# Kernel optimization log

Measured on AMD Instinct MI355X. Metric: run time of the kernel, lower is better.

Reference implementation:

```python
import jax, jax.numpy as jnp
import numpy as np

B, H, W, K, A = 4096, 32, 32, 20, 4


def setup_inputs() -> dict:
    key = jax.random.key(0)
    k_wall, k_agent, k_goal, k_phi, k_l1, k_l2 = jax.random.split(key, 6)
    # obs channels: 0 = wall/feature map (random), 1 = one-hot agent pos, 2 = one-hot goal pos
    walls = jax.random.uniform(k_wall, (B, H, W), dtype=jnp.float32)
    agent_idx = jax.random.randint(k_agent, (B,), 0, H * W)
    goal_idx = jax.random.randint(k_goal, (B,), 0, H * W)
    agent = jax.nn.one_hot(agent_idx, H * W, dtype=jnp.float32).reshape(B, H, W)
    goal = jax.nn.one_hot(goal_idx, H * W, dtype=jnp.float32).reshape(B, H, W)
    obs = jnp.stack([walls, agent, goal], axis=-1)  # (B,H,W,3)
    obs_flat = obs.reshape(B, H * W * 3)
    din = H * W * 3
    return {
        "obs_flat": obs_flat,
        "Phi_w": jax.random.normal(k_phi, (din, 2 * H * W), dtype=jnp.float32) * 0.02,
        "Phi_b": jnp.zeros((2 * H * W,), jnp.float32),
        "L1_w": jax.random.normal(k_l1, (36, 16), dtype=jnp.float32) * 0.1,
        "L1_b": jnp.zeros((16,), jnp.float32),
        "L2_w": jax.random.normal(k_l2, (16, A), dtype=jnp.float32) * 0.1,
        "L2_b": jnp.zeros((A,), jnp.float32),
    }


def _mvprop(r, p):
    # K-step value propagation: V <- max(V, r + p*(best 4-neighbor V - r))
    # p = sigmoid(...) >= 0, so max over the 4 shifted nv values equals nv of the max shift.
    def body(V, _):
        pv = jnp.pad(V, ((0, 0), (1, 1), (1, 1)))
        nbr = jnp.maximum(
            jnp.maximum(pv[:, :-2, 1:-1], pv[:, 2:, 1:-1]),   # up, down
            jnp.maximum(pv[:, 1:-1, :-2], pv[:, 1:-1, 2:]),   # left, right
        )
        return jnp.maximum(V, r + p * (nbr - r)), None
    V, _ = jax.lax.scan(body, r, None, length=K)
    return V


def reference(obs_flat, Phi_w, Phi_b, L1_w, L1_b, L2_w, L2_b):
    b = obs_flat.shape[0]
    obs = obs_flat.reshape(b, H, W, 3)
    phi = jax.nn.sigmoid(obs_flat @ Phi_w + Phi_b).reshape(b, H, W, 2)
    r, p = phi[..., 0], phi[..., 1]
    V = _mvprop(r, p)  # (b,H,W)
    obs_val = jnp.concatenate([obs, V[..., None]], axis=-1)  # (b,H,W,4)
    padded = jnp.pad(obs_val, ((0, 0), (1, 1), (1, 1), (0, 0)))
    # agent position: exactly one nonzero in channel 1 per sample -> argmax
    idx = jnp.argmax(obs[..., 1].reshape(b, -1), axis=1)
    pi, pj = idx // W, idx % W
    # 3x3 neighborhood around agent in padded grid (start = pos+1-1 = pos)
    def slice_one(ov, i, j):
        return jax.lax.dynamic_slice(ov, (i, j, 0), (3, 3, 4))
    sel = jax.vmap(slice_one)(padded, pi, pj)  # (b,3,3,4)
    h = jax.nn.relu(sel.reshape(b, 36) @ L1_w + L1_b)
    logit = h @ L2_w + L2_b
    return logit
```

## Files before the change

kernel.cpp:

```cpp
#include <hip/hip_runtime.h>
#include <hip/hip_fp16.h>

#define BATCH 4096
#define HH 32
#define WW 32
#define KPROP 20
#define NACT 4
#define DIN 3072
#define DPHI 2048
#define HWC 1024
#define KC 1024
#define TILE_ELEMS (16 * KC)

typedef _Float16 h8_t __attribute__((ext_vector_type(8)));
typedef _Float16 h4_t __attribute__((ext_vector_type(4)));
typedef float f32x4 __attribute__((ext_vector_type(4)));

__device__ inline float sigmoidf(float x) { return 1.0f / (1.0f + __expf(-x)); }

__device__ inline float dpp_shr1(float x) {
    return __int_as_float(__builtin_amdgcn_update_dpp(
        0, __float_as_int(x), 0x111, 0xF, 0xF, true));
}
__device__ inline float dpp_shl1(float x) {
    return __int_as_float(__builtin_amdgcn_update_dpp(
        0, __float_as_int(x), 0x101, 0xF, 0xF, true));
}

__device__ inline size_t pack_off(int row, int k) {
    return (size_t)(row >> 4) * TILE_ELEMS + (k >> 3) * 128 + (row & 15) * 8 + (k & 7);
}

__global__ __launch_bounds__(256) void prep_fused_kernel(
    const float* __restrict__ obs,
    const float* __restrict__ Phi_w,
    _Float16* __restrict__ A_pack,
    _Float16* __restrict__ B_pack,
    _Float16* __restrict__ Pag,
    int* __restrict__ aidx, int* __restrict__ gidx)
{
    if (blockIdx.x < BATCH) {
        const int t = blockIdx.x * 256 + threadIdx.x;
        const int b = t >> 8;
        const int c0 = (t & 255) * 4;
        const float* src = obs + (size_t)b * DIN + 3 * c0;
        const float4 f0 = *(const float4*)(src);
        const float4 f1 = *(const float4*)(src + 4);
        const float4 f2 = *(const float4*)(src + 8);
        h4_t w;
        w[0] = (_Float16)f0.x; w[1] = (_Float16)f0.w;
        w[2] = (_Float16)f1.z; w[3] = (_Float16)f2.y;
        *(h4_t*)(A_pack + pack_off(b, c0)) = w;
        if (f0.y > 0.5f) aidx[b] = c0;
        if (f1.x > 0.5f) aidx[b] = c0 + 1;
        if (f1.w > 0.5f) aidx[b] = c0 + 2;
        if (f2.z > 0.5f) aidx[b] = c0 + 3;
        if (f0.z > 0.5f) gidx[b] = c0;
        if (f1.y > 0.5f) gidx[b] = c0 + 1;
        if (f2.x > 0.5f) gidx[b] = c0 + 2;
        if (f2.w > 0.5f) gidx[b] = c0 + 3;
    } else {
        const int bid = blockIdx.x - BATCH;
        const int ni = bid & 63;
        const int ci = bid >> 6;
        const int tx = threadIdx.x & 31;
        const int ty = threadIdx.x >> 5;
        #pragma unroll
        for (int s = 0; s < 4; s++) {
            const int r = ty + 8 * s;
            const int c = ci * 32 + r;
            const int n = ni * 32 + tx;
            const float w0 = Phi_w[(size_t)(3 * c) * DPHI + n];
            Pag[(size_t)c * DPHI + n]         = (_Float16)Phi_w[(size_t)(3 * c + 1) * DPHI + n];
            Pag[(size_t)(HWC + c) * DPHI + n] = (_Float16)Phi_w[(size_t)(3 * c + 2) * DPHI + n];
            B_pack[pack_off(n, c)] = (_Float16)w0;
        }
    }
}

__global__ __launch_bounds__(256) void gemm_pre_kernel(
    const _Float16* __restrict__ A_pack,
    const _Float16* __restrict__ B_pack,
    const float* __restrict__ bias,
    _Float16* __restrict__ pre)
{
    __shared__ _Float16 As[4 * 8192];

    const int tid  = threadIdx.x;
    const int lane = tid & 63;
    const int wid  = tid >> 6;
    const int m0 = blockIdx.y * 64;
    const int n0 = blockIdx.x * 256 + wid * 64;
    const int lm = lane & 15;
    const int kq = lane >> 4;

    const _Float16* Apanel = A_pack + (size_t)(blockIdx.y * 4) * TILE_ELEMS;
    const _Float16* Bbase  = B_pack + (size_t)(blockIdx.x * 16 + wid * 4) * TILE_ELEMS + 8 * lane;

    f32x4 acc[4][4] = {};
    h8_t a0[4], a1[4], b0[4], b1[4];

    #define STAGE(H)                                                          \
        _Pragma("unroll")                                                     \
        for (int mt = 0; mt < 4; mt++)                                        \
            _Pragma("unroll")                                                 \
            for (int c = 0; c < 4; c++)                                       \
                __builtin_amdgcn_global_load_lds(                             \
                    (const __attribute__((address_space(1))) void*)           \
                        (Apanel + mt * TILE_ELEMS + (H) * 8192 + c * 2048 + tid * 8), \
                    (__attribute__((address_space(3))) void*)                 \
                        (As + mt * 8192 + c * 2048 + tid * 8), 16, 0, 0);

    #define AFRAG(AB, KL)                                                     \
        _Pragma("unroll")                                                     \
        for (int i = 0; i < 4; i++)                                           \
            AB[i] = *(const h8_t*)(As + i * 8192 + (KL) * 16 + 8 * lane);

    #define BFRAG(BB, KG)                                                     \
        _Pragma("unroll")                                                     \
        for (int i = 0; i < 4; i++)                                           \
            BB[i] = *(const h8_t*)(Bbase + i * TILE_ELEMS + (KG) * 16);

    #define COMPUTE(AB, BB)                                                   \
        _Pragma("unroll")                                                     \
        for (int mt = 0; mt < 4; mt++)                                        \
            _Pragma("unroll")                                                 \
            for (int nt = 0; nt < 4; nt++)                                    \
                acc[mt][nt] = __builtin_amdgcn_mfma_f32_16x16x32_f16(         \
                    AB[mt], BB[nt], acc[mt][nt], 0, 0, 0);

    STAGE(0);
    BFRAG(b0, 0); BFRAG(b1, 32);
    __syncthreads();

    #pragma unroll
    for (int h = 0; h < 2; h++) {
        if (h) { __syncthreads(); STAGE(1); __syncthreads(); }
        AFRAG(a0, 0); AFRAG(a1, 32);
        for (int kl = 0; kl < 512; kl += 64) {
            const int kg = h * 512 + kl;
            COMPUTE(a0, b0);
            if (kl + 64 < 512) { AFRAG(a0, kl + 64); }
            if (kg + 64 < KC)  { BFRAG(b0, kg + 64); }
            COMPUTE(a1, b1);
            if (kl + 96 < 512) { AFRAG(a1, kl + 96); }
            if (kg + 96 < KC)  { BFRAG(b1, kg + 96); }
        }
    }
    #undef STAGE
    #undef AFRAG
    #undef BFRAG
    #undef COMPUTE

    #pragma unroll
    for (int nt = 0; nt < 4; nt++) {
        const int col = n0 + nt * 16 + lm;
        const float bcol = bias[col];
        #pragma unroll
        for (int mt = 0; mt < 4; mt++) {
            #pragma unroll
            for (int r = 0; r < 4; r++) {
                const int row = m0 + mt * 16 + kq * 4 + r;
                pre[(size_t)row * DPHI + col] = (_Float16)(acc[mt][nt][r] + bcol);
            }
        }
    }
}

__global__ __launch_bounds__(256, 4) void vprop_head_kernel(
    const _Float16* __restrict__ pre,
    const _Float16* __restrict__ Pag,
    const float* __restrict__ obs,
    const int* __restrict__ aidx,
    const int* __restrict__ gidx,
    const float* __restrict__ L1w,
    const float* __restrict__ L1b,
    const float* __restrict__ L2w,
    const float* __restrict__ L2b,
    float* __restrict__ out)
{
    __shared__ __align__(16) float Vg[4][HWC];
    __shared__ float sel[4][36], hbuf[4][16];

    const int tid  = threadIdx.x;
    const int w    = tid >> 6;
    const int lane = tid & 63;
    const int b    = blockIdx.x * 4 + w;
    const int bi   = lane & 15;
    const int bj   = lane >> 4;
    const int ai = aidx[b];
    const int gi = gidx[b];

    const _Float16* pb = pre + (size_t)b * DPHI;
    const _Float16* ra = Pag + (size_t)ai * DPHI;
    const _Float16* rg = Pag + (size_t)(HWC + gi) * DPHI;

    float v[2][8], p[2][8], a[2][8];
    #pragma unroll
    for (int r = 0; r < 2; r++) {
        const int off = 64 * (2 * bi + r) + 16 * bj;
        const h8_t ph0 = *(const h8_t*)(pb + off), ph1 = *(const h8_t*)(pb + off + 8);
        const h8_t pa0 = *(const h8_t*)(ra + off), pa1 = *(const h8_t*)(ra + off + 8);
        const h8_t pg0 = *(const h8_t*)(rg + off), pg1 = *(const h8_t*)(rg + off + 8);
        #pragma unroll
        for (int c = 0; c < 4; c++) {
            const float rv = sigmoidf((float)ph0[2*c]   + (float)pa0[2*c]   + (float)pg0[2*c]);
            const float pv = sigmoidf((float)ph0[2*c+1] + (float)pa0[2*c+1] + (float)pg0[2*c+1]);
            v[r][c] = rv; p[r][c] = pv; a[r][c] = rv * (1.0f - pv);
            const float rv2 = sigmoidf((float)ph1[2*c]   + (float)pa1[2*c]   + (float)pg1[2*c]);
            const float pv2 = sigmoidf((float)ph1[2*c+1] + (float)pa1[2*c+1] + (float)pg1[2*c+1]);
            v[r][c+4] = rv2; p[r][c+4] = pv2; a[r][c+4] = rv2 * (1.0f - pv2);
        }
    }

    for (int it = 0; it < KPROP; it++) {
        float uh[8], dh[8], lh[2], rh[2];
        #pragma unroll
        for (int c = 0; c < 8; c++) {
            uh[c] = dpp_shr1(v[1][c]);
            dh[c] = dpp_shl1(v[0][c]);
        }
        #pragma unroll
        for (int r = 0; r < 2; r++) {
            lh[r] = __shfl(v[r][7], lane - 16);
            rh[r] = __shfl(v[r][0], lane + 16);
            if (bj == 0) lh[r] = 0.0f;
            if (bj == 3) rh[r] = 0.0f;
        }
        float nb[2][8];
        #pragma unroll
        for (int c = 0; c < 8; c++) {
            const float lf0 = (c == 0) ? lh[0] : v[0][c-1];
            const float rt0 = (c == 7) ? rh[0] : v[0][c+1];
            const float lf1 = (c == 0) ? lh[1] : v[1][c-1];
            const float rt1 = (c == 7) ? rh[1] : v[1][c+1];
            nb[0][c] = fmaxf(fmaxf(uh[c], v[1][c]), fmaxf(lf0, rt0));
            nb[1][c] = fmaxf(fmaxf(v[0][c], dh[c]), fmaxf(lf1, rt1));
        }
        #pragma unroll
        for (int r = 0; r < 2; r++)
            #pragma unroll
            for (int c = 0; c < 8; c++)
                v[r][c] = fmaxf(v[r][c], fmaf(p[r][c], nb[r][c], a[r][c]));
    }

    #pragma unroll
    for (int r = 0; r < 2; r++) {
        float4 lo, hi;
        lo.x = v[r][0]; lo.y = v[r][1]; lo.z = v[r][2]; lo.w = v[r][3];
        hi.x = v[r][4]; hi.y = v[r][5]; hi.z = v[r][6]; hi.w = v[r][7];
        const int base = (2 * bi + r) * 32 + 8 * bj;
        *(float4*)&Vg[w][base]     = lo;
        *(float4*)&Vg[w][base + 4] = hi;
    }
    __syncthreads();

    const int pi = ai >> 5, pj = ai & 31;
    if (lane < 36) {
        const int cell = lane >> 2;
        const int ch = lane & 3;
        const int di = pi + cell / 3 - 1;
        const int dj = pj + cell % 3 - 1;
        float vv = 0.0f;
        if (di >= 0 && di < HH && dj >= 0 && dj < WW) {
            const int c = di * WW + dj;
            vv = (ch < 3) ? obs[(size_t)b * DIN + 3 * c + ch] : Vg[w][c];
        }
        sel[w][lane] = vv;
    }
    __syncthreads();

    if (lane < 16) {
        float h = L1b[lane];
        #pragma unroll
        for (int k = 0; k < 36; k++) h += sel[w][k] * L1w[k * 16 + lane];
        hbuf[w][lane] = fmaxf(h, 0.0f);
    }
    __syncthreads();

    if (lane < 4) {
        float o = L2b[lane];
        #pragma unroll
        for (int t = 0; t < 16; t++) o += hbuf[w][t] * L2w[t * 4 + lane];
        out[(size_t)b * NACT + lane] = o;
    }
}

extern "C" void kernel_launch(void* const* d_in, const int* in_sizes, int n_in,
                              void* d_out, int out_size, void* d_ws, size_t ws_size,
                              hipStream_t stream) {
    const float* obs   = (const float*)d_in[0];
    const float* Phi_w = (const float*)d_in[1];
    const float* Phi_b = (const float*)d_in[2];
    const float* L1w   = (const float*)d_in[3];
    const float* L1b   = (const float*)d_in[4];
    const float* L2w   = (const float*)d_in[5];
    const float* L2b   = (const float*)d_in[6];
    float* out = (float*)d_out;

    char* ws = (char*)d_ws;
    _Float16* pre    = (_Float16*)ws;
    _Float16* A_pack = (_Float16*)(ws + 16777216);
    _Float16* B_pack = (_Float16*)(ws + 25165824);
    _Float16* Pag    = (_Float16*)(ws + 29360128);
    int* aidx = (int*)(ws + 37748736);
    int* gidx = aidx + BATCH;

    prep_fused_kernel<<<BATCH + 2048, 256, 0, stream>>>(obs, Phi_w, A_pack, B_pack, Pag, aidx, gidx);
    gemm_pre_kernel<<<dim3(8, 64), 256, 0, stream>>>(A_pack, B_pack, Phi_b, pre);
    vprop_head_kernel<<<BATCH / 4, 256, 0, stream>>>(pre, Pag, obs, aidx, gidx,
                                                     L1w, L1b, L2w, L2b, out);
}
```

Measured before the change: 166.6 us.

## Enlarge GEMM block to 128 rows with double-buffered LDS A staging

The feature GEMM now uses 512-thread blocks covering 128 rows by 256 columns, with two wave rows sharing each B column slice. A is staged into LDS in 128-wide K chunks with double buffering, so the next chunk's global-to-LDS copy overlaps the current chunk's MFMA work. This replaces the old scheme of two large half-K stages separated by full barriers. Fewer blocks (256 versus 512) may reduce occupancy and parallelism across the CUs, and there is now one barrier per chunk.

```diff
diff --git a/kernel.cpp b/kernel.cpp
--- a/kernel.cpp
+++ b/kernel.cpp
@@ -78,74 +78,77 @@
     }
 }
 
-__global__ __launch_bounds__(256) void gemm_pre_kernel(
+__global__ __launch_bounds__(512, 2) void gemm_pre_kernel(
     const _Float16* __restrict__ A_pack,
     const _Float16* __restrict__ B_pack,
     const float* __restrict__ bias,
     _Float16* __restrict__ pre)
 {
-    __shared__ _Float16 As[4 * 8192];
+    __shared__ __align__(16) _Float16 As[2 * 16384];
 
     const int tid  = threadIdx.x;
     const int lane = tid & 63;
     const int wid  = tid >> 6;
-    const int m0 = blockIdx.y * 64;
-    const int n0 = blockIdx.x * 256 + wid * 64;
+    const int wr   = wid >> 2;
+    const int wc   = wid & 3;
+    const int m0 = blockIdx.y * 128;
+    const int n0 = blockIdx.x * 256 + wc * 64;
     const int lm = lane & 15;
     const int kq = lane >> 4;
 
-    const _Float16* Apanel = A_pack + (size_t)(blockIdx.y * 4) * TILE_ELEMS;
-    const _Float16* Bbase  = B_pack + (size_t)(blockIdx.x * 16 + wid * 4) * TILE_ELEMS + 8 * lane;
+    const _Float16* Apanel = A_pack + (size_t)(blockIdx.y * 8) * TILE_ELEMS;
+    const _Float16* Bbase  = B_pack + (size_t)(blockIdx.x * 16 + wc * 4) * TILE_ELEMS + 8 * lane;
+
+    const int si = tid >> 6;
+    const int st = (tid & 63) * 8;
 
     f32x4 acc[4][4] = {};
     h8_t a0[4], a1[4], b0[4], b1[4];
 
-    #define STAGE(H)                                                          \
-        _Pragma("unroll")                                                     \
-        for (int mt = 0; mt < 4; mt++)                                        \
-            _Pragma("unroll")                                                 \
-            for (int c = 0; c < 4; c++)                                       \
-                __builtin_amdgcn_global_load_lds(                             \
-                    (const __attribute__((address_space(1))) void*)           \
-                        (Apanel + mt * TILE_ELEMS + (H) * 8192 + c * 2048 + tid * 8), \
-                    (__attribute__((address_space(3))) void*)                 \
-                        (As + mt * 8192 + c * 2048 + tid * 8), 16, 0, 0);
-
-    #define AFRAG(AB, KL)                                                     \
-        _Pragma("unroll")                                                     \
-        for (int i = 0; i < 4; i++)                                           \
-            AB[i] = *(const h8_t*)(As + i * 8192 + (KL) * 16 + 8 * lane);
-
-    #define BFRAG(BB, KG)                                                     \
-        _Pragma("unroll")                                                     \
-        for (int i = 0; i < 4; i++)                                           \
-            BB[i] = *(const h8_t*)(Bbase + i * TILE_ELEMS + (KG) * 16);
-
-    #define COMPUTE(AB, BB)                                                   \
-        _Pragma("unroll")                                                     \
-        for (int mt = 0; mt < 4; mt++)                                        \
-            _Pragma("unroll")                                                 \
-            for (int nt = 0; nt < 4; nt++)                                    \
-                acc[mt][nt] = __builtin_amdgcn_mfma_f32_16x16x32_f16(         \
+    #define STAGE(E)                                                           \
+        _Pragma("unroll")                                                      \
+        for (int c = 0; c < 4; c++)                                            \
+            __builtin_amdgcn_global_load_lds(                                  \
+                (const __attribute__((address_space(1))) void*)                \
+                    (Apanel + si * TILE_ELEMS + (E) * 2048 + c * 512 + st),    \
+                (__attribute__((address_space(3))) void*)                      \
+                    (As + ((E) & 1) * 16384 + si * 2048 + c * 512 + st), 16, 0, 0);
+
+    #define AFRAG(AB, E, KL)                                                   \
+        _Pragma("unroll")                                                      \
+        for (int i = 0; i < 4; i++)                                            \
+            AB[i] = *(const h8_t*)(As + ((E) & 1) * 16384 +                    \
+                                   (wr * 4 + i) * 2048 + (KL) * 16 + 8 * lane);
+
+    #define BFRAG(BB, KG)                                                      \
+        if ((KG) < KC) {                                                       \
+            _Pragma("unroll")                                                  \
+            for (int i = 0; i < 4; i++)                                        \
+                BB[i] = *(const h8_t*)(Bbase + i * TILE_ELEMS + (KG) * 16);    \
+        }
+
+    #define COMPUTE(AB, BB)                                                    \
+        _Pragma("unroll")                                                      \
+        for (int mt = 0; mt < 4; mt++)                                         \
+            _Pragma("unroll")                                                  \
+            for (int nt = 0; nt < 4; nt++)                                     \
+                acc[mt][nt] = __builtin_amdgcn_mfma_f32_16x16x32_f16(          \
                     AB[mt], BB[nt], acc[mt][nt], 0, 0, 0);
 
     STAGE(0);
     BFRAG(b0, 0); BFRAG(b1, 32);
     __syncthreads();
 
-    #pragma unroll
-    for (int h = 0; h < 2; h++) {
-        if (h) { __syncthreads(); STAGE(1); __syncthreads(); }
-        AFRAG(a0, 0); AFRAG(a1, 32);
-        for (int kl = 0; kl < 512; kl += 64) {
-            const int kg = h * 512 + kl;
-            COMPUTE(a0, b0);
-            if (kl + 64 < 512) { AFRAG(a0, kl + 64); }
-            if (kg + 64 < KC)  { BFRAG(b0, kg + 64); }
-            COMPUTE(a1, b1);
-            if (kl + 96 < 512) { AFRAG(a1, kl + 96); }
-            if (kg + 96 < KC)  { BFRAG(b1, kg + 96); }
-        }
+    #pragma unroll 1
+    for (int e = 0; e < 8; e++) {
+        const int kg0 = e * 128;
+        if (e < 7) STAGE(e + 1);
+        AFRAG(a0, e, 0); AFRAG(a1, e, 32);
+        COMPUTE(a0, b0); AFRAG(a0, e, 64);  BFRAG(b0, kg0 + 64);
+        COMPUTE(a1, b1); AFRAG(a1, e, 96);  BFRAG(b1, kg0 + 96);
+        COMPUTE(a0, b0);                    BFRAG(b0, kg0 + 128);
+        COMPUTE(a1, b1);                    BFRAG(b1, kg0 + 160);
+        __syncthreads();
     }
     #undef STAGE
     #undef AFRAG
@@ -160,7 +163,7 @@
         for (int mt = 0; mt < 4; mt++) {
             #pragma unroll
             for (int r = 0; r < 4; r++) {
-                const int row = m0 + mt * 16 + kq * 4 + r;
+                const int row = m0 + wr * 64 + mt * 16 + kq * 4 + r;
                 pre[(size_t)row * DPHI + col] = (_Float16)(acc[mt][nt][r] + bcol);
             }
         }
@@ -307,7 +310,7 @@
     int* gidx = aidx + BATCH;
 
     prep_fused_kernel<<<BATCH + 2048, 256, 0, stream>>>(obs, Phi_w, A_pack, B_pack, Pag, aidx, gidx);
-    gemm_pre_kernel<<<dim3(8, 64), 256, 0, stream>>>(A_pack, B_pack, Phi_b, pre);
+    gemm_pre_kernel<<<dim3(8, 32), 512, 0, stream>>>(A_pack, B_pack, Phi_b, pre);
     vprop_head_kernel<<<BATCH / 4, 256, 0, stream>>>(pre, Pag, obs, aidx, gidx,
                                                      L1w, L1b, L2w, L2b, out);
 }
```

Measured after the change: 170.3 us. 1.02x slower.
